# Kernel optimization log

Measured on AMD Instinct MI355X. Metric: run time of the kernel, lower is better.

Reference implementation:

```python
import jax, jax.numpy as jnp
import numpy as np

V, SMAX, D, H, L, DFF, W = 32000, 1024, 1024, 16, 2, 4096, 256
HD = D // H
EPS = 1e-6


def setup_inputs() -> dict:
    key = jax.random.key(0)
    ks = jax.random.split(key, 20)
    s = lambda k, shape, scale=0.02: jax.random.normal(k, shape, dtype=jnp.float32) * scale
    return {
        "input_ids": jax.random.randint(ks[0], (2, SMAX), 0, V, dtype=jnp.int64),
        "emb": s(ks[1], (V, D)),
        "pos": s(ks[2], (SMAX, D)),
        "norm1_w": jnp.ones((L, D), jnp.float32),
        "norm2_w": jnp.ones((L, D), jnp.float32),
        "wq": s(ks[3], (L, D, D)), "bq": jnp.zeros((L, D), jnp.float32),
        "wk": s(ks[4], (L, D, D)), "bk": jnp.zeros((L, D), jnp.float32),
        "wv": s(ks[5], (L, D, D)), "bv": jnp.zeros((L, D), jnp.float32),
        "wo": s(ks[6], (L, D, D)), "bo": jnp.zeros((L, D), jnp.float32),
        "w1": s(ks[7], (L, D, DFF)), "b1": jnp.zeros((L, DFF), jnp.float32),
        "w2": s(ks[8], (L, DFF, D)), "b2": jnp.zeros((L, D), jnp.float32),
        "normf_w": jnp.ones((D,), jnp.float32),
    }


def rms(x, w):
    return x * jax.lax.rsqrt(jnp.mean(x * x, axis=-1, keepdims=True) + EPS) * w


def reference(input_ids, emb, pos, norm1_w, norm2_w, wq, bq, wk, bk, wv, bv,
              wo, bo, w1, b1, w2, b2, normf_w):
    B, S = input_ids.shape
    x = emb[input_ids] + pos[:S]  # [B,S,D]
    # sliding-window causal mask: attend to j with 0 <= i-j < W
    i = jnp.arange(S)[:, None]
    j = jnp.arange(S)[None, :]
    mask = (j <= i) & (i - j < W)  # [S,S]
    neg = jnp.asarray(-1e9, x.dtype)
    for l in range(L):
        h = rms(x, norm1_w[l])
        q = (h @ wq[l] + bq[l]).reshape(B, S, H, HD)
        k = (h @ wk[l] + bk[l]).reshape(B, S, H, HD)
        v = (h @ wv[l] + bv[l]).reshape(B, S, H, HD)
        scores = jnp.einsum('bqhd,bkhd->bhqk', q, k) / np.sqrt(HD).astype(np.float32)
        scores = jnp.where(mask[None, None], scores, neg)
        attn = jax.nn.softmax(scores, axis=-1)
        o = jnp.einsum('bhqk,bkhd->bqhd', attn, v).reshape(B, S, D)
        x = x + (o @ wo[l] + bo[l])
        h2 = rms(x, norm2_w[l])
        x = x + (jax.nn.gelu(h2 @ w1[l] + b1[l], approximate=False) @ w2[l] + b2[l])
    x = rms(x, normf_w)
    logits = x @ emb.T  # tied lm_head
    return logits
```

## Files before the change

### kernel.cpp

```cpp
#include <hip/hip_runtime.h>
#include <hip/hip_bf16.h>
#include <cstdint>

typedef __bf16 bf16;
typedef __bf16 bf16x8 __attribute__((ext_vector_type(8)));
typedef __bf16 bf16x4 __attribute__((ext_vector_type(4)));
typedef float  f32x4  __attribute__((ext_vector_type(4)));

constexpr int V_    = 32000;
constexpr int SMAX_ = 1024;
constexpr int D_    = 1024;
constexpr int H_    = 16;
constexpr int L_    = 2;
constexpr int DFF_  = 4096;
constexpr int WIN_  = 256;
constexpr int B_    = 2;
constexpr int M_    = B_ * SMAX_;

#define SBAR0_() __builtin_amdgcn_sched_barrier(0)
#define HWBAR_() { __builtin_amdgcn_s_barrier(); SBAR0_(); }
#define LGKM0_() { asm volatile("s_waitcnt lgkmcnt(0)" ::: "memory"); SBAR0_(); }
#define VM0_()   { asm volatile("s_waitcnt vmcnt(0)" ::: "memory"); SBAR0_(); }

__global__ __launch_bounds__(512, 4) void gemm_lm8(
    const bf16* __restrict__ A, const bf16* __restrict__ BT,
    float* __restrict__ outf, int Nn)
{
  constexpr int KK = 1024, NT = 32;
  __shared__ __align__(16) bf16 ldsA[2][8192];
  __shared__ __align__(16) bf16 ldsB[2][4096];

  const int t = threadIdx.x, lane = t & 63, w = t >> 6;
  const int l16 = lane & 15, lh = lane >> 4;
  const int wm = w >> 1, wn = w & 1;

  const int nloc = gridDim.x >> 3;
  const int wg = (blockIdx.x & 7) * nloc + (blockIdx.x >> 3);
  const long m0 = (long)(wg & 7) * 256;
  const long n0 = (long)(wg >> 3) * 128;

  auto STGA = [&](int c, int k0) {
    #pragma unroll
    for (int q = 0; q < 2; ++q) {
      int row = q * 128 + (t >> 2);
      int sl  = (t & 3) ^ (row & 3);
      const bf16* g = A + (m0 + row) * (long)KK + k0 + sl * 8;
      __builtin_amdgcn_global_load_lds(
          (const __attribute__((address_space(1))) uint32_t*)g,
          (__attribute__((address_space(3))) uint32_t*)(&ldsA[c][q * 4096 + t * 8]),
          16, 0, 0);
    }
  };
  auto STGB = [&](int c, int k0) {
    int row = t >> 2;
    int sl  = (t & 3) ^ (row & 3);
    const bf16* g = BT + (n0 + row) * (long)KK + k0 + sl * 8;
    __builtin_amdgcn_global_load_lds(
        (const __attribute__((address_space(1))) uint32_t*)g,
        (__attribute__((address_space(3))) uint32_t*)(&ldsB[c][t * 8]),
        16, 0, 0);
  };
  auto LDA = [&](int c, int mi) -> bf16x8 {
    int row = wm * 64 + mi * 16 + l16;
    int sl  = lh ^ (row & 3);
    return *(const bf16x8*)(&ldsA[c][row * 32 + sl * 8]);
  };
  auto LDB = [&](int c, int ni) -> bf16x8 {
    int row = wn * 64 + ni * 16 + l16;
    int sl  = lh ^ (row & 3);
    return *(const bf16x8*)(&ldsB[c][row * 32 + sl * 8]);
  };

  f32x4 acc[4][4] = {};
  bf16x8 a[4], b[4];

  STGA(0, 0); STGB(0, 0);
  int kNext = 32;

  for (int j = 0; j < NT; ++j) {
    const int c = j & 1;
    VM0_();
    HWBAR_();
    #pragma unroll
    for (int mi = 0; mi < 4; ++mi) a[mi] = LDA(c, mi);
    #pragma unroll
    for (int ni = 0; ni < 4; ++ni) b[ni] = LDB(c, ni);
    STGA(c ^ 1, kNext); STGB(c ^ 1, kNext);
    LGKM0_();
    __builtin_amdgcn_s_setprio(1);
    #pragma unroll
    for (int mi = 0; mi < 4; ++mi)
      #pragma unroll
      for (int ni = 0; ni < 4; ++ni)
        acc[mi][ni] = __builtin_amdgcn_mfma_f32_16x16x32_bf16(b[ni], a[mi], acc[mi][ni], 0, 0, 0);
    __builtin_amdgcn_s_setprio(0);
    HWBAR_();
    kNext += 32; if (kNext == KK) kNext = 0;
  }

  asm volatile("s_waitcnt vmcnt(0) lgkmcnt(0)" ::: "memory");
  #pragma unroll
  for (int mi = 0; mi < 4; ++mi) {
    long row = m0 + wm * 64 + mi * 16 + l16;
    #pragma unroll
    for (int ni = 0; ni < 4; ++ni) {
      long col = n0 + wn * 64 + ni * 16 + lh * 4;
      *(f32x4*)(outf + row * Nn + col) = acc[mi][ni];
    }
  }
}

template<int BM, int EPI>
__global__ __launch_bounds__(256) void gemm_l2(
    const bf16* __restrict__ A, const bf16* __restrict__ BT,
    const float* __restrict__ bias, float* __restrict__ resid,
    bf16* __restrict__ outb, float* __restrict__ outf,
    int Nn, int Kk, int nbyMask, int nbyShift)
{
  constexpr int MR = BM / 32;
  constexpr int CA = BM / 32;
  __shared__ __align__(16) bf16 ldsA[2][BM * 64];
  __shared__ __align__(16) bf16 ldsB[2][8192];

  const int t = threadIdx.x, lane = t & 63, w = t >> 6;
  const int l16 = lane & 15, lh = lane >> 4;
  const int wm = w >> 1, wn = w & 1;

  const int nwg = gridDim.x, bid = blockIdx.x;
  const int nloc = nwg >> 3;
  const int wg = (bid & 7) * nloc + (bid >> 3);
  const long m0 = (long)(wg & nbyMask) * BM;
  const long n0 = (long)(wg >> nbyShift) * 128;

  auto STGA = [&](int c, int k0) {
    #pragma unroll
    for (int q = 0; q < CA; ++q) {
      int row = q * 32 + (t >> 3);
      int sl  = (t & 7) ^ (row & 7);
      const bf16* g = A + (m0 + row) * (long)Kk + k0 + sl * 8;
      __builtin_amdgcn_global_load_lds(
          (const __attribute__((address_space(1))) uint32_t*)g,
          (__attribute__((address_space(3))) uint32_t*)(&ldsA[c][q * 2048 + t * 8]),
          16, 0, 0);
    }
  };
  auto STGB = [&](int c, int k0) {
    #pragma unroll
    for (int q = 0; q < 4; ++q) {
      int row = q * 32 + (t >> 3);
      int sl  = (t & 7) ^ (row & 7);
      const bf16* g = BT + (n0 + row) * (long)Kk + k0 + sl * 8;
      __builtin_amdgcn_global_load_lds(
          (const __attribute__((address_space(1))) uint32_t*)g,
          (__attribute__((address_space(3))) uint32_t*)(&ldsB[c][q * 2048 + t * 8]),
          16, 0, 0);
    }
  };
  auto LDA = [&](int c, int mi, int ks) -> bf16x8 {
    int row = wm * (BM / 2) + mi * 16 + l16;
    int sl  = (ks * 4 + lh) ^ (row & 7);
    return *(const bf16x8*)(&ldsA[c][row * 64 + sl * 8]);
  };
  auto LDB = [&](int c, int ni, int ks) -> bf16x8 {
    int row = wn * 64 + ni * 16 + l16;
    int sl  = (ks * 4 + lh) ^ (row & 7);
    return *(const bf16x8*)(&ldsB[c][row * 64 + sl * 8]);
  };

  f32x4 acc[MR][4] = {};
  bf16x8 a[MR], b[4];

  STGA(0, 0); STGB(0, 0);
  int kNext = 64;

  const int NT = Kk >> 6;
  for (int j = 0; j < NT; ++j) {
    const int c = j & 1;
    VM0_();
    HWBAR_();
    #pragma unroll
    for (int mi = 0; mi < MR; ++mi) a[mi] = LDA(c, mi, 0);
    #pragma unroll
    for (int ni = 0; ni < 4; ++ni) b[ni] = LDB(c, ni, 0);
    STGA(c ^ 1, kNext); STGB(c ^ 1, kNext);
    LGKM0_();
    __builtin_amdgcn_s_setprio(1);
    #pragma unroll
    for (int mi = 0; mi < MR; ++mi)
      #pragma unroll
      for (int ni = 0; ni < 4; ++ni)
        acc[mi][ni] = __builtin_amdgcn_mfma_f32_16x16x32_bf16(b[ni], a[mi], acc[mi][ni], 0, 0, 0);
    __builtin_amdgcn_s_setprio(0);
    HWBAR_();
    #pragma unroll
    for (int mi = 0; mi < MR; ++mi) a[mi] = LDA(c, mi, 1);
    #pragma unroll
    for (int ni = 0; ni < 4; ++ni) b[ni] = LDB(c, ni, 1);
    LGKM0_();
    __builtin_amdgcn_s_setprio(1);
    #pragma unroll
    for (int mi = 0; mi < MR; ++mi)
      #pragma unroll
      for (int ni = 0; ni < 4; ++ni)
        acc[mi][ni] = __builtin_amdgcn_mfma_f32_16x16x32_bf16(b[ni], a[mi], acc[mi][ni], 0, 0, 0);
    __builtin_amdgcn_s_setprio(0);
    kNext += 64; if (kNext == Kk) kNext = 0;
  }

  #pragma unroll
  for (int mi = 0; mi < MR; ++mi) {
    long row = m0 + wm * (BM / 2) + mi * 16 + l16;
    #pragma unroll
    for (int ni = 0; ni < 4; ++ni) {
      long col = n0 + wn * 64 + ni * 16 + lh * 4;
      f32x4 v = acc[mi][ni];
      if (EPI == 3) {
        *(f32x4*)(outf + row * Nn + col) = v;
      } else {
        f32x4 bv = *(const f32x4*)(bias + col);
        v += bv;
        if (EPI == 0) {
          bf16x4 o;
          #pragma unroll
          for (int e = 0; e < 4; ++e) o[e] = (bf16)v[e];
          *(bf16x4*)(outb + row * Nn + col) = o;
        } else if (EPI == 1) {
          bf16x4 o;
          #pragma unroll
          for (int e = 0; e < 4; ++e) {
            float xx = v[e];
            o[e] = (bf16)(0.5f * xx * (1.0f + erff(xx * 0.70710678118654752f)));
          }
          *(bf16x4*)(outb + row * Nn + col) = o;
        } else {
          f32x4 r = *(f32x4*)(resid + row * Nn + col);
          r += v;
          *(f32x4*)(resid + row * Nn + col) = r;
        }
      }
    }
  }
}

__global__ __launch_bounds__(256) void attn_swa(
    const bf16* __restrict__ qkv, bf16* __restrict__ o)
{
  constexpr int PADK = 72;
  constexpr int PADV = 40;
  __shared__ bf16 Qs[64 * PADK];
  __shared__ bf16 Ks[32 * PADK];
  __shared__ bf16 Vt[64 * PADV];
  __shared__ bf16 Ps[4][16 * PADV];

  const int bid = blockIdx.x;
  const int qb = bid & 15;
  const int h  = (bid >> 4) & 15;
  const int b  = bid >> 8;
  const int q0 = qb * 64;
  const int t = threadIdx.x, lane = t & 63, w = t >> 6;
  const int l16 = lane & 15, lh = lane >> 4;

  #pragma unroll
  for (int i = 0; i < 2; i++) {
    int e = t + i * 256;
    int row = e >> 3, cc = e & 7;
    uint4 g = *(const uint4*)(qkv + ((long)(b * SMAX_ + q0 + row)) * 3072 + h * 64 + cc * 8);
    *(uint4*)(Qs + row * PADK + cc * 8) = g;
  }
  __syncthreads();
  bf16x8 aq[2];
  const int qrow = w * 16 + l16;
  #pragma unroll
  for (int ks = 0; ks < 2; ks++)
    aq[ks] = *(const bf16x8*)(Qs + qrow * PADK + ks * 32 + lh * 8);

  float m_run[4], l_run[4];
  f32x4 oacc[4];
  #pragma unroll
  for (int rr = 0; rr < 4; rr++) { m_run[rr] = -1e30f; l_run[rr] = 0.0f; }
  #pragma unroll
  for (int n = 0; n < 4; n++) oacc[n] = (f32x4){0.f, 0.f, 0.f, 0.f};

  const int tlo = q0 - (WIN_ - 1);
  const int jlo = (tlo <= 0) ? 0 : (tlo & ~31);
  const int iq  = q0 + w * 16 + lh * 4;

  for (int j0 = jlo; j0 < q0 + 64; j0 += 32) {
    __syncthreads();
    {
      int row = t >> 3, cc = t & 7;
      long base = ((long)(b * SMAX_ + j0 + row)) * 3072 + h * 64 + cc * 8;
      uint4 gk = *(const uint4*)(qkv + base + 1024);
      *(uint4*)(Ks + row * PADK + cc * 8) = gk;
      bf16x8 vv = *(const bf16x8*)(qkv + base + 2048);
      #pragma unroll
      for (int j = 0; j < 8; j++)
        Vt[(cc * 8 + j) * PADV + row] = vv[j];
    }
    __syncthreads();

    f32x4 s[2] = {(f32x4){0.f,0.f,0.f,0.f}, (f32x4){0.f,0.f,0.f,0.f}};
    #pragma unroll
    for (int nt = 0; nt < 2; nt++)
      #pragma unroll
      for (int ks = 0; ks < 2; ks++) {
        bf16x8 bk = *(const bf16x8*)(Ks + (nt * 16 + l16) * PADK + ks * 32 + lh * 8);
        s[nt] = __builtin_amdgcn_mfma_f32_16x16x32_bf16(aq[ks], bk, s[nt], 0, 0, 0);
      }

    float sc[2][4];
    #pragma unroll
    for (int nt = 0; nt < 2; nt++)
      #pragma unroll
      for (int rr = 0; rr < 4; rr++) {
        int i = iq + rr;
        int j = j0 + nt * 16 + l16;
        float v = s[nt][rr] * 0.125f;
        bool ok = (j <= i) && (i - j < WIN_);
        sc[nt][rr] = ok ? v : -1e30f;
      }

    float pb[2][4], alpha[4];
    #pragma unroll
    for (int rr = 0; rr < 4; rr++) {
      float mt = fmaxf(sc[0][rr], sc[1][rr]);
      #pragma unroll
      for (int off = 1; off < 16; off <<= 1) mt = fmaxf(mt, __shfl_xor(mt, off, 64));
      float mn = fmaxf(m_run[rr], mt);
      float a = __expf(m_run[rr] - mn);
      m_run[rr] = mn; alpha[rr] = a;
      float p0 = __expf(sc[0][rr] - mn);
      float p1 = __expf(sc[1][rr] - mn);
      pb[0][rr] = p0; pb[1][rr] = p1;
      float ls = p0 + p1;
      #pragma unroll
      for (int off = 1; off < 16; off <<= 1) ls += __shfl_xor(ls, off, 64);
      l_run[rr] = l_run[rr] * a + ls;
    }
    #pragma unroll
    for (int n = 0; n < 4; n++)
      #pragma unroll
      for (int rr = 0; rr < 4; rr++) oacc[n][rr] *= alpha[rr];

    #pragma unroll
    for (int rr = 0; rr < 4; rr++) {
      int prow = lh * 4 + rr;
      Ps[w][prow * PADV + l16]      = (bf16)pb[0][rr];
      Ps[w][prow * PADV + 16 + l16] = (bf16)pb[1][rr];
    }
    __syncthreads();

    bf16x8 pa = *(const bf16x8*)(&Ps[w][l16 * PADV + lh * 8]);
    #pragma unroll
    for (int n = 0; n < 4; n++) {
      bf16x8 bv = *(const bf16x8*)(Vt + (n * 16 + l16) * PADV + lh * 8);
      oacc[n] = __builtin_amdgcn_mfma_f32_16x16x32_bf16(pa, bv, oacc[n], 0, 0, 0);
    }
  }

  #pragma unroll
  for (int rr = 0; rr < 4; rr++) {
    int i = iq + rr;
    float inv = 1.0f / l_run[rr];
    #pragma unroll
    for (int n = 0; n < 4; n++)
      o[((long)(b * SMAX_ + i)) * D_ + h * 64 + n * 16 + l16] = (bf16)(oacc[n][rr] * inv);
  }
}

__global__ __launch_bounds__(256) void transpose_cvt(
    const float* __restrict__ src, bf16* __restrict__ dst,
    int Kk, int Nn, long srcL, long dstL)
{
  __shared__ float tile[32][33];
  const int tx = threadIdx.x, ty = threadIdx.y;
  const long n0 = (long)blockIdx.x * 32, k0 = (long)blockIdx.y * 32;
  src += (long)blockIdx.z * srcL;
  dst += (long)blockIdx.z * dstL;
  #pragma unroll
  for (int i = 0; i < 4; i++)
    tile[ty + i * 8][tx] = src[(k0 + ty + i * 8) * Nn + n0 + tx];
  __syncthreads();
  #pragma unroll
  for (int i = 0; i < 4; i++)
    dst[(n0 + ty + i * 8) * Kk + k0 + tx] = (bf16)tile[tx][ty + i * 8];
}

__global__ __launch_bounds__(256) void cvt_bf16(
    const float* __restrict__ src, bf16* __restrict__ dst, long n4)
{
  long i = (long)blockIdx.x * 256 + threadIdx.x;
  if (i >= n4) return;
  float4 v = ((const float4*)src)[i];
  bf16x4 o; o[0] = (bf16)v.x; o[1] = (bf16)v.y; o[2] = (bf16)v.z; o[3] = (bf16)v.w;
  ((bf16x4*)dst)[i] = o;
}

__global__ __launch_bounds__(256) void pack_bqkv(
    const float* __restrict__ bq, const float* __restrict__ bk,
    const float* __restrict__ bv, float* __restrict__ out)
{
  int i = blockIdx.x * 256 + threadIdx.x;
  if (i >= L_ * 3072) return;
  int l = i / 3072, c = i % 3072;
  float v = (c < 1024) ? bq[l * 1024 + c]
          : (c < 2048) ? bk[l * 1024 + c - 1024]
                       : bv[l * 1024 + c - 2048];
  out[i] = v;
}

__global__ __launch_bounds__(256) void embed_k(
    const int* __restrict__ ids, const float* __restrict__ emb,
    const float* __restrict__ pos, float* __restrict__ x)
{
  const int m = blockIdx.x, t = threadIdx.x;
  const int id = ids[m];
  const int s = m & (SMAX_ - 1);
  float4 e = ((const float4*)(emb + (long)id * D_))[t];
  float4 p = ((const float4*)(pos + (long)s * D_))[t];
  float4 rr; rr.x = e.x + p.x; rr.y = e.y + p.y; rr.z = e.z + p.z; rr.w = e.w + p.w;
  ((float4*)(x + (long)m * D_))[t] = rr;
}

__global__ __launch_bounds__(256) void rmsnorm_k(
    const float* __restrict__ x, const float* __restrict__ wgt,
    bf16* __restrict__ out)
{
  __shared__ float red[4];
  const int m = blockIdx.x, t = threadIdx.x;
  float4 v = ((const float4*)(x + (long)m * D_))[t];
  float ss = v.x * v.x + v.y * v.y + v.z * v.z + v.w * v.w;
  #pragma unroll
  for (int off = 1; off < 64; off <<= 1) ss += __shfl_xor(ss, off, 64);
  const int lane = t & 63, w = t >> 6;
  if (lane == 0) red[w] = ss;
  __syncthreads();
  float tot = red[0] + red[1] + red[2] + red[3];
  float rs = rsqrtf(tot * (1.0f / D_) + 1e-6f);
  float4 g = ((const float4*)wgt)[t];
  bf16x4 o;
  o[0] = (bf16)(v.x * rs * g.x); o[1] = (bf16)(v.y * rs * g.y);
  o[2] = (bf16)(v.z * rs * g.z); o[3] = (bf16)(v.w * rs * g.w);
  ((bf16x4*)(out + (long)m * D_))[t] = o;
}

extern "C" void kernel_launch(void* const* d_in, const int* in_sizes, int n_in,
                              void* d_out, int out_size, void* d_ws, size_t ws_size,
                              hipStream_t stream)
{
  const int*   ids = (const int*)d_in[0];
  const float* emb = (const float*)d_in[1];
  const float* pos = (const float*)d_in[2];
  const float* n1w = (const float*)d_in[3];
  const float* n2w = (const float*)d_in[4];
  const float* wq  = (const float*)d_in[5];
  const float* bq  = (const float*)d_in[6];
  const float* wk  = (const float*)d_in[7];
  const float* bk  = (const float*)d_in[8];
  const float* wv  = (const float*)d_in[9];
  const float* bv  = (const float*)d_in[10];
  const float* wo  = (const float*)d_in[11];
  const float* bo  = (const float*)d_in[12];
  const float* w1  = (const float*)d_in[13];
  const float* b1  = (const float*)d_in[14];
  const float* w2  = (const float*)d_in[15];
  const float* b2  = (const float*)d_in[16];
  const float* nfw = (const float*)d_in[17];

  char* p = (char*)d_ws;
  auto alloc = [&](size_t bytes) {
    char* rr = p; p += (bytes + 255) & ~(size_t)255; return rr;
  };
  bf16*  wqkv_t = (bf16*) alloc((size_t)L_ * 3 * 1024 * 1024 * 2);
  bf16*  wo_t   = (bf16*) alloc((size_t)L_ * 1024 * 1024 * 2);
  bf16*  w1_t   = (bf16*) alloc((size_t)L_ * 4096 * 1024 * 2);
  bf16*  w2_t   = (bf16*) alloc((size_t)L_ * 1024 * 4096 * 2);
  bf16*  emb_bf = (bf16*) alloc((size_t)V_ * D_ * 2);
  float* bqkv   = (float*)alloc((size_t)L_ * 3072 * 4);
  float* x      = (float*)alloc((size_t)M_ * D_ * 4);
  bf16*  hbuf   = (bf16*) alloc((size_t)M_ * D_ * 2);
  bf16*  qkv    = (bf16*) alloc((size_t)M_ * 3072 * 2);
  bf16*  obuf   = (bf16*) alloc((size_t)M_ * D_ * 2);
  bf16*  ff     = (bf16*) alloc((size_t)M_ * DFF_ * 2);

  const dim3 b32(32, 8, 1);
  transpose_cvt<<<dim3(32, 32, L_),  b32, 0, stream>>>(wq, wqkv_t,                1024, 1024, 1024 * 1024, 3 * 1024 * 1024);
  transpose_cvt<<<dim3(32, 32, L_),  b32, 0, stream>>>(wk, wqkv_t + 1024 * 1024,  1024, 1024, 1024 * 1024, 3 * 1024 * 1024);
  transpose_cvt<<<dim3(32, 32, L_),  b32, 0, stream>>>(wv, wqkv_t + 2*1024*1024,  1024, 1024, 1024 * 1024, 3 * 1024 * 1024);
  transpose_cvt<<<dim3(32, 32, L_),  b32, 0, stream>>>(wo, wo_t,                  1024, 1024, 1024 * 1024, 1024 * 1024);
  transpose_cvt<<<dim3(128, 32, L_), b32, 0, stream>>>(w1, w1_t,                  1024, 4096, 1024 * 4096, 4096 * 1024);
  transpose_cvt<<<dim3(32, 128, L_), b32, 0, stream>>>(w2, w2_t,                  4096, 1024, 4096 * 1024, 1024 * 4096);
  cvt_bf16<<<32000, 256, 0, stream>>>(emb, emb_bf, (long)V_ * D_ / 4);
  pack_bqkv<<<24, 256, 0, stream>>>(bq, bk, bv, bqkv);
  embed_k<<<M_, 256, 0, stream>>>(ids, emb, pos, x);

  for (int l = 0; l < L_; l++) {
    rmsnorm_k<<<M_, 256, 0, stream>>>(x, n1w + l * D_, hbuf);
    gemm_l2<64, 0><<<dim3(32 * 24), 256, 0, stream>>>(
        hbuf, wqkv_t + (size_t)l * 3 * 1024 * 1024, bqkv + l * 3072,
        nullptr, qkv, nullptr, 3072, 1024, 31, 5);
    attn_swa<<<B_ * H_ * (SMAX_ / 64), 256, 0, stream>>>(qkv, obuf);
    gemm_l2<64, 2><<<dim3(32 * 8), 256, 0, stream>>>(
        obuf, wo_t + (size_t)l * 1024 * 1024, bo + l * D_,
        x, nullptr, nullptr, 1024, 1024, 31, 5);
    rmsnorm_k<<<M_, 256, 0, stream>>>(x, n2w + l * D_, hbuf);
    gemm_l2<128, 1><<<dim3(16 * 32), 256, 0, stream>>>(
        hbuf, w1_t + (size_t)l * 4096 * 1024, b1 + l * DFF_,
        nullptr, ff, nullptr, 4096, 1024, 15, 4);
    gemm_l2<64, 2><<<dim3(32 * 8), 256, 0, stream>>>(
        ff, w2_t + (size_t)l * 1024 * 4096, b2 + l * D_,
        x, nullptr, nullptr, 1024, 4096, 31, 5);
  }
  rmsnorm_k<<<M_, 256, 0, stream>>>(x, nfw, hbuf);
  gemm_lm8<<<dim3(8 * (V_ / 128)), 512, 0, stream>>>(
      hbuf, emb_bf, (float*)d_out, V_);
}
```

Baseline: 631.8 us.

## Enlarge LM-head GEMM tile to 256x256 with four-stage LDS pipeline

Rewrites the tied LM-head GEMM kernel to compute 256x256 output tiles per workgroup instead of 256x128. Each wave now holds 8x4 accumulator tiles. Global-to-LDS loads move from double buffering to a four-stage ring with a partial vmcnt wait, and the trailing barrier is dropped. The aim is more operand reuse per loaded byte and more latency hiding for the global loads. In exchange, occupancy drops to one 512-thread block per CU (128KB LDS, many more accumulator registers), and the grid shrinks to 1000 blocks.

```diff
diff --git a/kernel.cpp b/kernel.cpp
--- a/kernel.cpp
+++ b/kernel.cpp
@@ -21,87 +21,78 @@
 #define HWBAR_() { __builtin_amdgcn_s_barrier(); SBAR0_(); }
 #define LGKM0_() { asm volatile("s_waitcnt lgkmcnt(0)" ::: "memory"); SBAR0_(); }
 #define VM0_()   { asm volatile("s_waitcnt vmcnt(0)" ::: "memory"); SBAR0_(); }
-
-__global__ __launch_bounds__(512, 4) void gemm_lm8(
+#define VM8_()   { asm volatile("s_waitcnt vmcnt(8)" ::: "memory"); SBAR0_(); }
+
+__global__ __launch_bounds__(512, 1) void gemm_lmA(
     const bf16* __restrict__ A, const bf16* __restrict__ BT,
     float* __restrict__ outf, int Nn)
 {
-  constexpr int KK = 1024, NT = 32;
-  __shared__ __align__(16) bf16 ldsA[2][8192];
-  __shared__ __align__(16) bf16 ldsB[2][4096];
+  constexpr int KK = 1024, NT = KK / 32;
+  __shared__ __align__(16) bf16 ldsA[4 * 8192];
+  __shared__ __align__(16) bf16 ldsB[4 * 8192];
 
   const int t = threadIdx.x, lane = t & 63, w = t >> 6;
   const int l16 = lane & 15, lh = lane >> 4;
-  const int wm = w >> 1, wn = w & 1;
+  const int wm = w >> 2, wn = w & 3;
 
   const int nloc = gridDim.x >> 3;
   const int wg = (blockIdx.x & 7) * nloc + (blockIdx.x >> 3);
   const long m0 = (long)(wg & 7) * 256;
-  const long n0 = (long)(wg >> 3) * 128;
-
-  auto STGA = [&](int c, int k0) {
-    #pragma unroll
-    for (int q = 0; q < 2; ++q) {
-      int row = q * 128 + (t >> 2);
-      int sl  = (t & 3) ^ (row & 3);
-      const bf16* g = A + (m0 + row) * (long)KK + k0 + sl * 8;
+  const long n0 = (long)(wg >> 3) * 256;
+
+  auto STG = [&](const bf16* src, long rowBase, bf16* dst, int k0) {
+    #pragma unroll
+    for (int j = 0; j < 2; ++j) {
+      int p = j * 8192 + t * 16;
+      int row = p >> 6;
+      int sl = ((p >> 4) & 3) ^ (row & 3);
+      const bf16* g = src + (rowBase + row) * (long)KK + k0 + sl * 8;
       __builtin_amdgcn_global_load_lds(
           (const __attribute__((address_space(1))) uint32_t*)g,
-          (__attribute__((address_space(3))) uint32_t*)(&ldsA[c][q * 4096 + t * 8]),
+          (__attribute__((address_space(3))) uint32_t*)(dst + j * 4096 + w * 512),
           16, 0, 0);
     }
   };
-  auto STGB = [&](int c, int k0) {
-    int row = t >> 2;
-    int sl  = (t & 3) ^ (row & 3);
-    const bf16* g = BT + (n0 + row) * (long)KK + k0 + sl * 8;
-    __builtin_amdgcn_global_load_lds(
-        (const __attribute__((address_space(1))) uint32_t*)g,
-        (__attribute__((address_space(3))) uint32_t*)(&ldsB[c][t * 8]),
-        16, 0, 0);
-  };
-  auto LDA = [&](int c, int mi) -> bf16x8 {
-    int row = wm * 64 + mi * 16 + l16;
-    int sl  = lh ^ (row & 3);
-    return *(const bf16x8*)(&ldsA[c][row * 32 + sl * 8]);
-  };
-  auto LDB = [&](int c, int ni) -> bf16x8 {
-    int row = wn * 64 + ni * 16 + l16;
-    int sl  = lh ^ (row & 3);
-    return *(const bf16x8*)(&ldsB[c][row * 32 + sl * 8]);
-  };
-
-  f32x4 acc[4][4] = {};
-  bf16x8 a[4], b[4];
-
-  STGA(0, 0); STGB(0, 0);
-  int kNext = 32;
-
-  for (int j = 0; j < NT; ++j) {
-    const int c = j & 1;
-    VM0_();
+  auto LDF = [&](const bf16* base, int rowb) -> bf16x8 {
+    int row = rowb + l16;
+    return *(const bf16x8*)(base + row * 32 + ((lh ^ (l16 & 3)) << 3));
+  };
+
+  f32x4 acc[8][4] = {};
+
+  STG(A, m0, ldsA,          0);  STG(BT, n0, ldsB,          0);
+  STG(A, m0, ldsA + 8192,  32);  STG(BT, n0, ldsB + 8192,  32);
+  STG(A, m0, ldsA + 16384, 64);  STG(BT, n0, ldsB + 16384, 64);
+  int kNext = 96;
+
+  for (int i = 0; i < NT; ++i) {
+    const int cur = i & 3, nb = (i + 3) & 3;
+    VM8_();
     HWBAR_();
-    #pragma unroll
-    for (int mi = 0; mi < 4; ++mi) a[mi] = LDA(c, mi);
-    #pragma unroll
-    for (int ni = 0; ni < 4; ++ni) b[ni] = LDB(c, ni);
-    STGA(c ^ 1, kNext); STGB(c ^ 1, kNext);
+    const bf16* Ac = ldsA + cur * 8192;
+    const bf16* Bc = ldsB + cur * 8192;
+    bf16x8 af[8], bb[4];
+    #pragma unroll
+    for (int mi = 0; mi < 8; ++mi) af[mi] = LDF(Ac, wm * 128 + mi * 16);
+    #pragma unroll
+    for (int ni = 0; ni < 4; ++ni) bb[ni] = LDF(Bc, wn * 64 + ni * 16);
+    STG(A, m0, ldsA + nb * 8192, kNext);
+    STG(BT, n0, ldsB + nb * 8192, kNext);
+    kNext += 32; if (kNext == KK) kNext = 0;
     LGKM0_();
     __builtin_amdgcn_s_setprio(1);
     #pragma unroll
-    for (int mi = 0; mi < 4; ++mi)
+    for (int mi = 0; mi < 8; ++mi)
       #pragma unroll
       for (int ni = 0; ni < 4; ++ni)
-        acc[mi][ni] = __builtin_amdgcn_mfma_f32_16x16x32_bf16(b[ni], a[mi], acc[mi][ni], 0, 0, 0);
+        acc[mi][ni] = __builtin_amdgcn_mfma_f32_16x16x32_bf16(bb[ni], af[mi], acc[mi][ni], 0, 0, 0);
     __builtin_amdgcn_s_setprio(0);
-    HWBAR_();
-    kNext += 32; if (kNext == KK) kNext = 0;
   }
 
   asm volatile("s_waitcnt vmcnt(0) lgkmcnt(0)" ::: "memory");
   #pragma unroll
-  for (int mi = 0; mi < 4; ++mi) {
-    long row = m0 + wm * 64 + mi * 16 + l16;
+  for (int mi = 0; mi < 8; ++mi) {
+    long row = m0 + wm * 128 + mi * 16 + l16;
     #pragma unroll
     for (int ni = 0; ni < 4; ++ni) {
       long col = n0 + wn * 64 + ni * 16 + lh * 4;
@@ -512,6 +503,6 @@
         x, nullptr, nullptr, 1024, 4096, 31, 5);
   }
   rmsnorm_k<<<M_, 256, 0, stream>>>(x, nfw, hbuf);
-  gemm_lm8<<<dim3(8 * (V_ / 128)), 512, 0, stream>>>(
+  gemm_lmA<<<dim3(8 * (V_ / 256)), 512, 0, stream>>>(
       hbuf, emb_bf, (float*)d_out, V_);
 }
```

New measurement: 620.6 us. About the same (-1.8%).
